# Kernel optimization log

Hardware: AMD Instinct MI355X
Metric: run time of the kernel (lower is better)

Reference implementation:

```python
import jax, jax.numpy as jnp
import numpy as np

D_MODEL = 1024
N_HEADS = 16
D_K = D_MODEL // N_HEADS
D_FF = 4096
EPS = 1e-6


def setup_inputs() -> dict:
    key = jax.random.key(0)
    ks = jax.random.split(key, 8)
    s = 0.02
    return {
        "x": jax.random.normal(ks[0], (2, 2048, D_MODEL), dtype=jnp.float32),
        "Wq": jax.random.normal(ks[1], (D_MODEL, D_MODEL), dtype=jnp.float32) * s,
        "bq": jnp.zeros((D_MODEL,), jnp.float32),
        "Wk": jax.random.normal(ks[2], (D_MODEL, D_MODEL), dtype=jnp.float32) * s,
        "bk": jnp.zeros((D_MODEL,), jnp.float32),
        "Wv": jax.random.normal(ks[3], (D_MODEL, D_MODEL), dtype=jnp.float32) * s,
        "bv": jnp.zeros((D_MODEL,), jnp.float32),
        "Wo": jax.random.normal(ks[4], (D_MODEL, D_MODEL), dtype=jnp.float32) * s,
        "bo": jnp.zeros((D_MODEL,), jnp.float32),
        "W1": jax.random.normal(ks[5], (D_FF, D_MODEL), dtype=jnp.float32) * s,
        "b1": jnp.zeros((D_FF,), jnp.float32),
        "W2": jax.random.normal(ks[6], (D_MODEL, D_FF), dtype=jnp.float32) * s,
        "b2": jnp.zeros((D_MODEL,), jnp.float32),
        "g1": jnp.ones((D_MODEL,), jnp.float32),
        "be1": jnp.zeros((D_MODEL,), jnp.float32),
        "g2": jnp.ones((D_MODEL,), jnp.float32),
        "be2": jnp.zeros((D_MODEL,), jnp.float32),
    }


def _layernorm(x, gamma, beta):
    mean = x.mean(axis=-1, keepdims=True)
    var = ((x - mean) ** 2).mean(axis=-1, keepdims=True)
    return gamma * (x - mean) / jnp.sqrt(var + EPS) + beta


def _linear(x, W, b):
    # torch nn.Linear: y = x @ W.T + b
    return x @ W.T + b


def reference(x, Wq, bq, Wk, bk, Wv, bv, Wo, bo, W1, b1, W2, b2, g1, be1, g2, be2):
    B, S, _ = x.shape
    h = _layernorm(x, g1, be1)
    # project and split heads -> [B, H, S, d_k]
    Q = _linear(h, Wq, bq).reshape(B, S, N_HEADS, D_K).transpose(0, 2, 1, 3)
    K = _linear(h, Wk, bk).reshape(B, S, N_HEADS, D_K).transpose(0, 2, 1, 3)
    V = _linear(h, Wv, bv).reshape(B, S, N_HEADS, D_K).transpose(0, 2, 1, 3)
    scores = jnp.einsum("bhqd,bhkd->bhqk", Q, K) / jnp.sqrt(jnp.float32(D_K))
    attn = jax.nn.softmax(scores, axis=-1)
    ctx = jnp.einsum("bhqk,bhkd->bhqd", attn, V)
    ctx = ctx.transpose(0, 2, 1, 3).reshape(B, S, D_MODEL)
    x = x + _linear(ctx, Wo, bo)
    h2 = _layernorm(x, g2, be2)
    ff = _linear(jax.nn.gelu(_linear(h2, W1, b1), approximate=False), W2, b2)
    return x + ff
```

## Files before the change

kernel.cpp:

```cpp
#include <hip/hip_runtime.h>
#include <stdint.h>

#define D_MODEL 1024
#define N_HEADS 16
#define DKH     64
#define D_FF    4096
#define BATCH   2
#define SEQ     2048
#define M_TOK   (BATCH*SEQ)

typedef unsigned short u16;
typedef __attribute__((ext_vector_type(8))) short short8;
typedef __attribute__((ext_vector_type(4))) float f32x4;

__device__ __forceinline__ u16 f2b(float f){
  union { float f; uint32_t i; } c; c.f = f;
  uint32_t x = c.i;
  uint32_t r = x + 0x7fffu + ((x >> 16) & 1u);
  return (u16)(r >> 16);
}

__device__ __forceinline__ uint32_t pk_bf16(float a, float b){
  uint32_t d;
  asm("v_cvt_pk_bf16_f32 %0, %1, %2" : "=v"(d) : "v"(a), "v"(b));
  return d;
}

__device__ __forceinline__ void gl_lds16(const u16* g, u16* l){
  __builtin_amdgcn_global_load_lds(
      (const __attribute__((address_space(1))) void*)g,
      (__attribute__((address_space(3))) void*)l, 16, 0, 0);
}

#define MFMA16(a,b,c) __builtin_amdgcn_mfma_f32_16x16x32_bf16((a),(b),(c),0,0,0)

__global__ __launch_bounds__(256) void cvt6_kernel(
    const float* __restrict__ s0, const float* __restrict__ s1,
    const float* __restrict__ s2, const float* __restrict__ s3,
    const float* __restrict__ s4, const float* __restrict__ s5,
    u16* __restrict__ d0, u16* __restrict__ d1, u16* __restrict__ d2,
    u16* __restrict__ d3, u16* __restrict__ d4, u16* __restrict__ d5)
{
  const float* s; u16* d; int n;
  switch (blockIdx.y){
    case 0: s=s0; d=d0; n=D_MODEL*D_MODEL; break;
    case 1: s=s1; d=d1; n=D_MODEL*D_MODEL; break;
    case 2: s=s2; d=d2; n=D_MODEL*D_MODEL; break;
    case 3: s=s3; d=d3; n=D_MODEL*D_MODEL; break;
    case 4: s=s4; d=d4; n=D_FF*D_MODEL;   break;
    default: s=s5; d=d5; n=D_MODEL*D_FF;  break;
  }
  int i = (blockIdx.x * 256 + threadIdx.x) * 4;
  if (i < n){
    float4 f = *(const float4*)&s[i];
    ushort4 o; o.x = f2b(f.x); o.y = f2b(f.y); o.z = f2b(f.z); o.w = f2b(f.w);
    *(ushort4*)&d[i] = o;
  }
}

__global__ __launch_bounds__(256) void ln_kernel(
    const float* __restrict__ X, const float* __restrict__ G,
    const float* __restrict__ Bt, u16* __restrict__ O)
{
  const int row = blockIdx.x;
  const int t = threadIdx.x;
  float4 xv = *(const float4*)&X[(size_t)row * D_MODEL + t * 4];
  float s  = xv.x + xv.y + xv.z + xv.w;
  float s2 = xv.x*xv.x + xv.y*xv.y + xv.z*xv.z + xv.w*xv.w;
  #pragma unroll
  for (int off = 32; off >= 1; off >>= 1){
    s  += __shfl_down(s,  off, 64);
    s2 += __shfl_down(s2, off, 64);
  }
  __shared__ float psum[4], psum2[4];
  const int wv = t >> 6, ln = t & 63;
  if (ln == 0){ psum[wv] = s; psum2[wv] = s2; }
  __syncthreads();
  float ts  = psum[0] + psum[1] + psum[2] + psum[3];
  float ts2 = psum2[0] + psum2[1] + psum2[2] + psum2[3];
  float mean = ts * (1.f / D_MODEL);
  float var  = ts2 * (1.f / D_MODEL) - mean * mean;
  float rstd = rsqrtf(var + 1e-6f);
  float4 g4 = *(const float4*)&G[t * 4];
  float4 b4 = *(const float4*)&Bt[t * 4];
  ushort4 o;
  o.x = f2b(g4.x * (xv.x - mean) * rstd + b4.x);
  o.y = f2b(g4.y * (xv.y - mean) * rstd + b4.y);
  o.z = f2b(g4.z * (xv.z - mean) * rstd + b4.z);
  o.w = f2b(g4.w * (xv.w - mean) * rstd + b4.w);
  *(ushort4*)&O[(size_t)row * D_MODEL + t * 4] = o;
}

template<int EPI, int OUTF, int TM>
__global__ __launch_bounds__(256,2) void gemm_bt(
    const u16* __restrict__ A, const u16* __restrict__ W,
    const float* __restrict__ bias, const float* resid,
    void* Cout, int K, int Ndim)
{
  constexpr int MI = TM / 32;
  __shared__ __align__(16) u16 sA[TM*64];
  __shared__ __align__(16) u16 sB[128*64];
  const int t = threadIdx.x;
  const int w = t >> 6, lane = t & 63, lr = lane & 15, quad = lane >> 4;
  const int wm = (w & 1) * (TM/2), wn = (w >> 1) * 64;
  const int m0 = blockIdx.y * TM, n0 = blockIdx.x * 128;
  const int srow = lane >> 3;
  const int scol = ((lane & 7) ^ srow) * 8;

  f32x4 acc[MI][4];
  #pragma unroll
  for (int i = 0; i < MI; i++)
    #pragma unroll
    for (int j = 0; j < 4; j++) acc[i][j] = (f32x4){0.f,0.f,0.f,0.f};

  for (int k0 = 0; k0 < K; k0 += 64){
    __syncthreads();
    #pragma unroll
    for (int it = 0; it < TM/32; it++)
      gl_lds16(&A[(size_t)(m0 + it*32 + w*8 + srow) * K + k0 + scol], &sA[(it*32 + w*8) * 64]);
    #pragma unroll
    for (int it = 0; it < 4; it++)
      gl_lds16(&W[(size_t)(n0 + it*32 + w*8 + srow) * K + k0 + scol], &sB[(it*32 + w*8) * 64]);
    __syncthreads();
    #pragma unroll
    for (int ks = 0; ks < 2; ks++){
      short8 af[MI], bfr[4];
      #pragma unroll
      for (int i = 0; i < MI; i++)
        af[i]  = *(const short8*)&sA[(wm + i*16 + lr)*64 + (((ks*4 + quad) ^ (lr & 7)) * 8)];
      #pragma unroll
      for (int j = 0; j < 4; j++)
        bfr[j] = *(const short8*)&sB[(wn + j*16 + lr)*64 + (((ks*4 + quad) ^ (lr & 7)) * 8)];
      #pragma unroll
      for (int i = 0; i < MI; i++)
        #pragma unroll
        for (int j = 0; j < 4; j++)
          acc[i][j] = MFMA16(af[i], bfr[j], acc[i][j]);
    }
  }

  #pragma unroll
  for (int j = 0; j < 4; j++){
    int gn = n0 + wn + j*16 + lr;
    float bb = bias[gn];
    #pragma unroll
    for (int i = 0; i < MI; i++){
      #pragma unroll
      for (int r = 0; r < 4; r++){
        int gm = m0 + wm + i*16 + quad*4 + r;
        size_t idx = (size_t)gm * Ndim + gn;
        float v = acc[i][j][r] + bb;
        if (EPI == 1){
          float p = v * (1.59576912f + 0.07135481f * v * v);
          float e = __builtin_amdgcn_exp2f(-1.44269504f * p);
          v = v * __builtin_amdgcn_rcpf(1.f + e);
        }
        if (EPI == 2) v += resid[idx];
        if (OUTF) ((float*)Cout)[idx] = v;
        else      ((u16*)Cout)[idx] = f2b(v);
      }
    }
  }
}

__global__ __launch_bounds__(256,2) void gemm_qkv(
    const u16* __restrict__ A,
    const u16* __restrict__ Wq, const float* __restrict__ bq,
    const u16* __restrict__ Wk, const float* __restrict__ bk,
    const u16* __restrict__ Wv, const float* __restrict__ bv,
    u16* __restrict__ Qo, u16* __restrict__ Ko, u16* __restrict__ Vo)
{
  __shared__ __align__(16) u16 sA[128*64];
  __shared__ __align__(16) u16 sB[128*64];
  const u16* W; const float* bias; u16* out; float scale;
  if (blockIdx.z == 0){ W = Wq; bias = bq; out = Qo; scale = 0.125f * 1.44269504f; }
  else if (blockIdx.z == 1){ W = Wk; bias = bk; out = Ko; scale = 1.f; }
  else { W = Wv; bias = bv; out = Vo; scale = 1.f; }

  const int t = threadIdx.x;
  const int w = t >> 6, lane = t & 63, lr = lane & 15, quad = lane >> 4;
  const int wm = (w & 1) * 64, wn = (w >> 1) * 64;
  const int m0 = blockIdx.y * 128, n0 = blockIdx.x * 128;
  const int srow = lane >> 3;
  const int scol = ((lane & 7) ^ srow) * 8;
  const int K = D_MODEL;

  f32x4 acc[4][4];
  #pragma unroll
  for (int i = 0; i < 4; i++)
    #pragma unroll
    for (int j = 0; j < 4; j++) acc[i][j] = (f32x4){0.f,0.f,0.f,0.f};

  for (int k0 = 0; k0 < K; k0 += 64){
    __syncthreads();
    #pragma unroll
    for (int it = 0; it < 4; it++){
      gl_lds16(&A[(size_t)(m0 + it*32 + w*8 + srow) * K + k0 + scol], &sA[(it*32 + w*8) * 64]);
      gl_lds16(&W[(size_t)(n0 + it*32 + w*8 + srow) * K + k0 + scol], &sB[(it*32 + w*8) * 64]);
    }
    __syncthreads();
    #pragma unroll
    for (int ks = 0; ks < 2; ks++){
      short8 af[4], bfr[4];
      #pragma unroll
      for (int i = 0; i < 4; i++)
        af[i]  = *(const short8*)&sA[(wm + i*16 + lr)*64 + (((ks*4 + quad) ^ (lr & 7)) * 8)];
      #pragma unroll
      for (int j = 0; j < 4; j++)
        bfr[j] = *(const short8*)&sB[(wn + j*16 + lr)*64 + (((ks*4 + quad) ^ (lr & 7)) * 8)];
      #pragma unroll
      for (int i = 0; i < 4; i++)
        #pragma unroll
        for (int j = 0; j < 4; j++)
          acc[i][j] = MFMA16(af[i], bfr[j], acc[i][j]);
    }
  }

  #pragma unroll
  for (int j = 0; j < 4; j++){
    int gn = n0 + wn + j*16 + lr;
    int hh = gn >> 6, d = gn & 63;
    float bb = bias[gn];
    #pragma unroll
    for (int i = 0; i < 4; i++){
      #pragma unroll
      for (int r = 0; r < 4; r++){
        int gm = m0 + wm + i*16 + quad*4 + r;
        int b = gm >> 11, sq = gm & 2047;
        float v = (acc[i][j][r] + bb) * scale;
        out[(((size_t)(b * N_HEADS + hh)) * SEQ + sq) * DKH + d] = f2b(v);
      }
    }
  }
}

__global__ __launch_bounds__(256) void transpose_v(
    const u16* __restrict__ V, u16* __restrict__ Vt)
{
  __shared__ __align__(16) u16 st[64][72];
  const int s0 = blockIdx.x * 64, bh = blockIdx.y, t = threadIdx.x;
  const u16* vp = V + (size_t)bh * SEQ * DKH;
  u16* op = Vt + (size_t)bh * DKH * SEQ;
  #pragma unroll
  for (int it = 0; it < 2; it++){
    int c = it * 256 + t, r = c >> 3, cc = c & 7;
    *(float4*)&st[r][cc*8] = *(const float4*)&vp[(size_t)(s0 + r) * DKH + cc*8];
  }
  __syncthreads();
  #pragma unroll
  for (int it = 0; it < 2; it++){
    int c = it * 256 + t, d = c >> 3, sc = c & 7;
    u16 tmp[8];
    #pragma unroll
    for (int e = 0; e < 8; e++) tmp[e] = st[sc*8 + e][d];
    float4 f; __builtin_memcpy(&f, tmp, 16);
    *(float4*)&op[(size_t)d * SEQ + s0 + sc*8] = f;
  }
}

__global__ __launch_bounds__(256,2) void attn_kernel(
    const u16* __restrict__ Q, const u16* __restrict__ K,
    const u16* __restrict__ Vt, u16* __restrict__ ctx)
{
  __shared__ __align__(16) u16 sK[128][72];
  __shared__ __align__(16) u16 sVt[64][136];
  __shared__ __align__(16) u16 sP[4][32][136];

  const int t = threadIdx.x, w = t >> 6, lane = t & 63;
  const int lr = lane & 15, quad = lane >> 4;
  const int q0 = blockIdx.x * 128;
  const int bh = blockIdx.y;
  const u16* Qp = Q + ((size_t)bh * SEQ + q0) * DKH;
  const u16* Kp = K + (size_t)bh * SEQ * DKH;
  const u16* Vp = Vt + (size_t)bh * DKH * SEQ;

  short8 qf[2][2];
  #pragma unroll
  for (int i = 0; i < 2; i++)
    #pragma unroll
    for (int ks = 0; ks < 2; ks++)
      qf[i][ks] = *(const short8*)&Qp[(size_t)(w*32 + i*16 + lr) * DKH + ks*32 + quad*8];

  short8 ones;
  #pragma unroll
  for (int e = 0; e < 8; e++) ones[e] = (short)0x3F80;

  f32x4 acco[2][4];
  f32x4 accl[2];
  #pragma unroll
  for (int i = 0; i < 2; i++){
    accl[i] = (f32x4){0.f,0.f,0.f,0.f};
    #pragma unroll
    for (int jc = 0; jc < 4; jc++) acco[i][jc] = (f32x4){0.f,0.f,0.f,0.f};
  }

  for (int kt = 0; kt < SEQ/128; kt++){
    const int s0 = kt * 128;
    __syncthreads();
    #pragma unroll
    for (int it = 0; it < 4; it++){
      int c = it * 256 + t, r = c >> 3, cc = c & 7;
      *(float4*)&sK[r][cc*8] = *(const float4*)&Kp[(size_t)(s0 + r) * DKH + cc*8];
    }
    #pragma unroll
    for (int it = 0; it < 4; it++){
      int c = it * 256 + t, d = c >> 4, sc = c & 15;
      *(float4*)&sVt[d][sc*8] = *(const float4*)&Vp[(size_t)d * SEQ + s0 + sc*8];
    }
    __syncthreads();

    f32x4 st_[2][8];
    #pragma unroll
    for (int i = 0; i < 2; i++)
      #pragma unroll
      for (int j = 0; j < 8; j++) st_[i][j] = (f32x4){0.f,0.f,0.f,0.f};
    #pragma unroll
    for (int ks = 0; ks < 2; ks++){
      #pragma unroll
      for (int j = 0; j < 8; j++){
        short8 kf = *(const short8*)&sK[j*16 + lr][ks*32 + quad*8];
        st_[0][j] = MFMA16(kf, qf[0][ks], st_[0][j]);
        st_[1][j] = MFMA16(kf, qf[1][ks], st_[1][j]);
      }
    }

    #pragma unroll
    for (int i = 0; i < 2; i++)
      #pragma unroll
      for (int j = 0; j < 8; j++){
        float p0 = __builtin_amdgcn_exp2f(st_[i][j][0]);
        float p1 = __builtin_amdgcn_exp2f(st_[i][j][1]);
        float p2 = __builtin_amdgcn_exp2f(st_[i][j][2]);
        float p3 = __builtin_amdgcn_exp2f(st_[i][j][3]);
        uint2 pv; pv.x = pk_bf16(p0, p1); pv.y = pk_bf16(p2, p3);
        *(uint2*)&sP[w][i*16 + lr][j*16 + quad*4] = pv;
      }

    #pragma unroll
    for (int ks = 0; ks < 4; ks++){
      short8 pf0 = *(const short8*)&sP[w][lr     ][ks*32 + quad*8];
      short8 pf1 = *(const short8*)&sP[w][16 + lr][ks*32 + quad*8];
      accl[0] = MFMA16(pf0, ones, accl[0]);
      accl[1] = MFMA16(pf1, ones, accl[1]);
      #pragma unroll
      for (int jc = 0; jc < 4; jc++){
        short8 vf = *(const short8*)&sVt[jc*16 + lr][ks*32 + quad*8];
        acco[0][jc] = MFMA16(pf0, vf, acco[0][jc]);
        acco[1][jc] = MFMA16(pf1, vf, acco[1][jc]);
      }
    }
  }

  const int bq = bh >> 4, hh = bh & 15;
  u16* op = ctx + ((size_t)bq * SEQ + q0) * D_MODEL + hh * DKH;
  #pragma unroll
  for (int i = 0; i < 2; i++){
    #pragma unroll
    for (int r = 0; r < 4; r++){
      float rl = 1.f / accl[i][r];
      int row = w*32 + i*16 + quad*4 + r;
      #pragma unroll
      for (int jc = 0; jc < 4; jc++)
        op[(size_t)row * D_MODEL + jc*16 + lr] = f2b(acco[i][jc][r] * rl);
    }
  }
}

extern "C" void kernel_launch(void* const* d_in, const int* in_sizes, int n_in,
                              void* d_out, int out_size, void* d_ws, size_t ws_size,
                              hipStream_t stream)
{
  const float* x   = (const float*)d_in[0];
  const float* Wq  = (const float*)d_in[1];
  const float* bq  = (const float*)d_in[2];
  const float* Wk  = (const float*)d_in[3];
  const float* bk  = (const float*)d_in[4];
  const float* Wv  = (const float*)d_in[5];
  const float* bv  = (const float*)d_in[6];
  const float* Wo  = (const float*)d_in[7];
  const float* bo  = (const float*)d_in[8];
  const float* W1  = (const float*)d_in[9];
  const float* b1  = (const float*)d_in[10];
  const float* W2  = (const float*)d_in[11];
  const float* b2  = (const float*)d_in[12];
  const float* g1  = (const float*)d_in[13];
  const float* be1 = (const float*)d_in[14];
  const float* g2  = (const float*)d_in[15];
  const float* be2 = (const float*)d_in[16];

  char* ws = (char*)d_ws;
  const size_t MB = 1024ull * 1024ull;
  u16* wqb = (u16*)(ws + 0*MB);
  u16* wkb = (u16*)(ws + 2*MB);
  u16* wvb = (u16*)(ws + 4*MB);
  u16* wob = (u16*)(ws + 6*MB);
  u16* w1b = (u16*)(ws + 8*MB);
  u16* w2b = (u16*)(ws + 16*MB);
  u16* h   = (u16*)(ws + 24*MB);
  u16* q   = (u16*)(ws + 32*MB);
  u16* k   = (u16*)(ws + 40*MB);
  u16* v   = (u16*)(ws + 48*MB);
  u16* vt  = (u16*)(ws + 56*MB);
  u16* ff  = (u16*)(ws + 32*MB);
  u16* ctx = v;
  u16* h2  = h;
  float* x1 = (float*)d_out;

  cvt6_kernel<<<dim3(4096, 6), 256, 0, stream>>>(
      Wq, Wk, Wv, Wo, W1, W2, wqb, wkb, wvb, wob, w1b, w2b);

  ln_kernel<<<M_TOK, 256, 0, stream>>>(x, g1, be1, h);
  gemm_qkv<<<dim3(D_MODEL/128, M_TOK/128, 3), 256, 0, stream>>>(
      h, wqb, bq, wkb, bk, wvb, bv, q, k, v);
  transpose_v<<<dim3(SEQ/64, BATCH*N_HEADS), 256, 0, stream>>>(v, vt);
  attn_kernel<<<dim3(SEQ/128, BATCH*N_HEADS), 256, 0, stream>>>(q, k, vt, ctx);
  gemm_bt<2,1,64><<<dim3(D_MODEL/128, M_TOK/64), 256, 0, stream>>>(
      ctx, wob, bo, x, (void*)x1, D_MODEL, D_MODEL);
  ln_kernel<<<M_TOK, 256, 0, stream>>>(x1, g2, be2, h2);
  gemm_bt<1,0,128><<<dim3(D_FF/128, M_TOK/128), 256, 0, stream>>>(
      h2, w1b, b1, nullptr, (void*)ff, D_MODEL, D_FF);
  gemm_bt<2,1,64><<<dim3(D_MODEL/128, M_TOK/64), 256, 0, stream>>>(
      ff, w2b, b2, x1, d_out, D_FF, D_MODEL);
}
```

Measured before the change: 358.9 us.

## Fuse first layernorm into weight-convert launch and swap grid axes for locality

Merges the first layernorm into the weight-conversion kernel as an extra grid row (blockIdx.y==6), which removes one launch. It also swaps the grid x/y mapping in the GEMM and attention kernels so consecutive blocks walk the M (token) or head dimension first. With M varying fastest, co-resident blocks share the same weight column tile, and attention blocks for one query tile across heads are grouped together. The intent is to change L2/MALL reuse patterns. The trade is that neighbouring blocks now share weight tiles rather than activation rows, which may lower or raise cache hit rates.

Measured after the change: 350.6 us. 2.3% less time.

```diff
diff --git a/kernel.cpp b/kernel.cpp
--- a/kernel.cpp
+++ b/kernel.cpp
@@ -34,13 +34,45 @@
 
 #define MFMA16(a,b,c) __builtin_amdgcn_mfma_f32_16x16x32_bf16((a),(b),(c),0,0,0)
 
-__global__ __launch_bounds__(256) void cvt6_kernel(
+__global__ __launch_bounds__(256) void cvt_ln_kernel(
     const float* __restrict__ s0, const float* __restrict__ s1,
     const float* __restrict__ s2, const float* __restrict__ s3,
     const float* __restrict__ s4, const float* __restrict__ s5,
     u16* __restrict__ d0, u16* __restrict__ d1, u16* __restrict__ d2,
-    u16* __restrict__ d3, u16* __restrict__ d4, u16* __restrict__ d5)
-{
+    u16* __restrict__ d3, u16* __restrict__ d4, u16* __restrict__ d5,
+    const float* __restrict__ X, const float* __restrict__ G,
+    const float* __restrict__ Bt, u16* __restrict__ O)
+{
+  __shared__ float psum[4], psum2[4];
+  if (blockIdx.y == 6){
+    const int row = blockIdx.x;
+    const int t = threadIdx.x;
+    float4 xv = *(const float4*)&X[(size_t)row * D_MODEL + t * 4];
+    float s  = xv.x + xv.y + xv.z + xv.w;
+    float s2 = xv.x*xv.x + xv.y*xv.y + xv.z*xv.z + xv.w*xv.w;
+    #pragma unroll
+    for (int off = 32; off >= 1; off >>= 1){
+      s  += __shfl_down(s,  off, 64);
+      s2 += __shfl_down(s2, off, 64);
+    }
+    const int wv = t >> 6, ln = t & 63;
+    if (ln == 0){ psum[wv] = s; psum2[wv] = s2; }
+    __syncthreads();
+    float ts  = psum[0] + psum[1] + psum[2] + psum[3];
+    float ts2 = psum2[0] + psum2[1] + psum2[2] + psum2[3];
+    float mean = ts * (1.f / D_MODEL);
+    float var  = ts2 * (1.f / D_MODEL) - mean * mean;
+    float rstd = rsqrtf(var + 1e-6f);
+    float4 g4 = *(const float4*)&G[t * 4];
+    float4 b4 = *(const float4*)&Bt[t * 4];
+    ushort4 o;
+    o.x = f2b(g4.x * (xv.x - mean) * rstd + b4.x);
+    o.y = f2b(g4.y * (xv.y - mean) * rstd + b4.y);
+    o.z = f2b(g4.z * (xv.z - mean) * rstd + b4.z);
+    o.w = f2b(g4.w * (xv.w - mean) * rstd + b4.w);
+    *(ushort4*)&O[(size_t)row * D_MODEL + t * 4] = o;
+    return;
+  }
   const float* s; u16* d; int n;
   switch (blockIdx.y){
     case 0: s=s0; d=d0; n=D_MODEL*D_MODEL; break;
@@ -103,7 +135,7 @@
   const int t = threadIdx.x;
   const int w = t >> 6, lane = t & 63, lr = lane & 15, quad = lane >> 4;
   const int wm = (w & 1) * (TM/2), wn = (w >> 1) * 64;
-  const int m0 = blockIdx.y * TM, n0 = blockIdx.x * 128;
+  const int m0 = blockIdx.x * TM, n0 = blockIdx.y * 128;
   const int srow = lane >> 3;
   const int scol = ((lane & 7) ^ srow) * 8;
 
@@ -180,7 +212,7 @@
   const int t = threadIdx.x;
   const int w = t >> 6, lane = t & 63, lr = lane & 15, quad = lane >> 4;
   const int wm = (w & 1) * 64, wn = (w >> 1) * 64;
-  const int m0 = blockIdx.y * 128, n0 = blockIdx.x * 128;
+  const int m0 = blockIdx.x * 128, n0 = blockIdx.y * 128;
   const int srow = lane >> 3;
   const int scol = ((lane & 7) ^ srow) * 8;
   const int K = D_MODEL;
@@ -268,8 +300,8 @@
 
   const int t = threadIdx.x, w = t >> 6, lane = t & 63;
   const int lr = lane & 15, quad = lane >> 4;
-  const int q0 = blockIdx.x * 128;
-  const int bh = blockIdx.y;
+  const int bh = blockIdx.x;
+  const int q0 = blockIdx.y * 128;
   const u16* Qp = Q + ((size_t)bh * SEQ + q0) * DKH;
   const u16* Kp = K + (size_t)bh * SEQ * DKH;
   const u16* Vp = Vt + (size_t)bh * DKH * SEQ;
@@ -406,19 +438,19 @@
   u16* h2  = h;
   float* x1 = (float*)d_out;
 
-  cvt6_kernel<<<dim3(4096, 6), 256, 0, stream>>>(
-      Wq, Wk, Wv, Wo, W1, W2, wqb, wkb, wvb, wob, w1b, w2b);
-
-  ln_kernel<<<M_TOK, 256, 0, stream>>>(x, g1, be1, h);
-  gemm_qkv<<<dim3(D_MODEL/128, M_TOK/128, 3), 256, 0, stream>>>(
+  cvt_ln_kernel<<<dim3(4096, 7), 256, 0, stream>>>(
+      Wq, Wk, Wv, Wo, W1, W2, wqb, wkb, wvb, wob, w1b, w2b,
+      x, g1, be1, h);
+
+  gemm_qkv<<<dim3(M_TOK/128, D_MODEL/128, 3), 256, 0, stream>>>(
       h, wqb, bq, wkb, bk, wvb, bv, q, k, v);
   transpose_v<<<dim3(SEQ/64, BATCH*N_HEADS), 256, 0, stream>>>(v, vt);
-  attn_kernel<<<dim3(SEQ/128, BATCH*N_HEADS), 256, 0, stream>>>(q, k, vt, ctx);
-  gemm_bt<2,1,64><<<dim3(D_MODEL/128, M_TOK/64), 256, 0, stream>>>(
+  attn_kernel<<<dim3(BATCH*N_HEADS, SEQ/128), 256, 0, stream>>>(q, k, vt, ctx);
+  gemm_bt<2,1,64><<<dim3(M_TOK/64, D_MODEL/128), 256, 0, stream>>>(
       ctx, wob, bo, x, (void*)x1, D_MODEL, D_MODEL);
   ln_kernel<<<M_TOK, 256, 0, stream>>>(x1, g2, be2, h2);
-  gemm_bt<1,0,128><<<dim3(D_FF/128, M_TOK/128), 256, 0, stream>>>(
+  gemm_bt<1,0,128><<<dim3(M_TOK/128, D_FF/128), 256, 0, stream>>>(
       h2, w1b, b1, nullptr, (void*)ff, D_MODEL, D_FF);
-  gemm_bt<2,1,64><<<dim3(D_MODEL/128, M_TOK/64), 256, 0, stream>>>(
+  gemm_bt<2,1,64><<<dim3(M_TOK/64, D_MODEL/128), 256, 0, stream>>>(
       ff, w2b, b2, x1, d_out, D_FF, D_MODEL);
 }
```
